# Performance work log

Measured on AMD Instinct MI355X. Metric: run time of the kernel, lower is better.

## Reference

```python
import jax, jax.numpy as jnp
import numpy as np

B, T, F, U = 64, 512, 1024, 256


def setup_inputs() -> dict:
    key = jax.random.key(0)
    ks = jax.random.split(key, 9)
    x = jax.random.normal(ks[0], (B, T, F), dtype=jnp.float32)
    # variable-length sequences, zero-padded tail (Masking layer semantics)
    lengths = jax.random.randint(ks[1], (B,), T // 2, T + 1)
    valid = (jnp.arange(T)[None, :] < lengths[:, None]).astype(jnp.float32)
    x = x * valid[:, :, None]
    s_fc = 1.0 / np.sqrt(F)
    s_u = 1.0 / np.sqrt(U)
    W_fc = jax.random.uniform(ks[2], (F, U), jnp.float32, -s_fc, s_fc)
    b_fc = jnp.zeros((U,), jnp.float32)
    W_x = jax.random.uniform(ks[3], (U, 4 * U), jnp.float32, -s_u, s_u)
    W_h = jax.random.uniform(ks[4], (U, 4 * U), jnp.float32, -s_u, s_u)
    # Keras unit_forget_bias: ones for forget-gate slice, zeros elsewhere
    b_lstm = jnp.concatenate([jnp.zeros((U,)), jnp.ones((U,)), jnp.zeros((2 * U,))]).astype(jnp.float32)
    W_p = jax.random.uniform(ks[5], (U, 1), jnp.float32, -s_u, s_u)
    b_p = jnp.zeros((1,), jnp.float32)
    return {"inputs": x, "W_fc": W_fc, "b_fc": b_fc, "W_x": W_x,
            "W_h": W_h, "b_lstm": b_lstm, "W_p": W_p, "b_p": b_p}


def _forward(inputs, W_fc, b_fc, W_x, W_h, b_lstm, W_p, b_p):
    # Masking layer: timestep masked iff ALL features == 0.0
    mask = jnp.any(inputs != 0.0, axis=-1)              # [B, T] bool
    x = inputs * mask[:, :, None].astype(inputs.dtype)  # Masking zeroes masked steps
    # Dense(units, relu) applied per timestep
    z = jax.nn.relu(jnp.einsum('btf,fu->btu', x, W_fc) + b_fc)  # [B, T, U]

    units = W_h.shape[0]
    h0 = jnp.zeros((x.shape[0], units), x.dtype)
    c0 = jnp.zeros((x.shape[0], units), x.dtype)

    def step(carry, xt_mt):
        h, c = carry
        xt, mt = xt_mt                                   # [B, U], [B]
        gates = xt @ W_x + h @ W_h + b_lstm              # [B, 4U]
        i, f, g, o = jnp.split(gates, 4, axis=-1)
        i = jax.nn.sigmoid(i)
        f = jax.nn.sigmoid(f)
        g = jnp.tanh(g)
        o = jax.nn.sigmoid(o)
        c_new = f * c + i * g
        h_new = o * jnp.tanh(c_new)
        m = mt[:, None]
        # Keras masked-RNN semantics: skip step, carry previous h/c and output
        h2 = jnp.where(m, h_new, h)
        c2 = jnp.where(m, c_new, c)
        return (h2, c2), h2

    z_t = jnp.swapaxes(z, 0, 1)        # [T, B, U]
    m_t = jnp.swapaxes(mask, 0, 1)     # [T, B]
    _, hs = jax.lax.scan(step, (h0, c0), (z_t, m_t))
    hs = jnp.swapaxes(hs, 0, 1)        # [B, T, U]
    # Dense(1, sigmoid) prediction head
    return jax.nn.sigmoid(jnp.einsum('btu,uo->bto', hs, W_p) + b_p)  # [B, T, 1]


def reference(inputs, W_fc, b_fc, W_x, W_h, b_lstm, W_p, b_p):
    return _forward(inputs, W_fc, b_fc, W_x, W_h, b_lstm, W_p, b_p)
```

## Files before the change

### kernel.cpp

```cpp
#include <hip/hip_runtime.h>
#include <hip/hip_fp16.h>
#include <hip/hip_fp8.h>
#include <cstdint>

#define BB 64
#define TT 512
#define FF 1024
#define UU 256
#define GG 1024

typedef _Float16 f16x8 __attribute__((ext_vector_type(8)));
typedef float f32x4 __attribute__((ext_vector_type(4)));
typedef int i32x8 __attribute__((ext_vector_type(8)));

typedef union { uint4 u4[2]; i32x8 v; } pk32;

__device__ __forceinline__ float sigmf_(float x) { return 1.f / (1.f + __expf(-x)); }
__device__ __forceinline__ float tanhf_(float x) { return 1.f - 2.f / (1.f + __expf(2.f * x)); }

__global__ __launch_bounds__(256) void mask_kernel(const float* __restrict__ x,
                                                   float* __restrict__ maskF) {
  int row = blockIdx.x;
  int tid = threadIdx.x;
  const float4* xr = (const float4*)(x + (size_t)row * FF);
  float4 v = xr[tid];
  bool nz = (v.x != 0.f) || (v.y != 0.f) || (v.z != 0.f) || (v.w != 0.f);
  __shared__ int flag;
  if (tid == 0) flag = 0;
  __syncthreads();
  if (__any(nz)) {
    if ((tid & 63) == 0) atomicOr(&flag, 1);
  }
  __syncthreads();
  if (tid == 0) maskF[row] = flag ? 1.f : 0.f;
}

__global__ __launch_bounds__(256) void pack_whP(const float* __restrict__ Wh,
                                                uint8_t* __restrict__ whP) {
  int col = blockIdx.x;
  int k = threadIdx.x;
  __hip_fp8_e4m3 f(Wh[(size_t)k * GG + col] * 16.f);
  whP[col * 256 + k] = (uint8_t)f.__x;
}

template <typename TA, bool RELU, bool PERM>
__global__ __launch_bounds__(256) void gemm16(const TA* __restrict__ A,
                                              const float* __restrict__ Bm,
                                              const float* __restrict__ bias,
                                              __half* __restrict__ C,
                                              int M, int N, int K) {
  __shared__ _Float16 As[128][40];
  __shared__ _Float16 Bs[64][40];
  int tid = threadIdx.x;
  int lane = tid & 63, w = tid >> 6;
  int wm = w & 1, wn = w >> 1;
  int m0 = blockIdx.x * 128, n0 = blockIdx.y * 64;
  int fr = lane & 15, ks = lane >> 4;

  f32x4 acc[4][2];
#pragma unroll
  for (int i = 0; i < 4; ++i)
#pragma unroll
    for (int j = 0; j < 2; ++j) acc[i][j] = (f32x4){0.f, 0.f, 0.f, 0.f};

  for (int k0 = 0; k0 < K; k0 += 32) {
    {
      int r = tid >> 3, kq = (tid & 7) * 4;
#pragma unroll
      for (int i = 0; i < 4; ++i) {
        int row = r + 32 * i;
        const TA* src = A + (size_t)(m0 + row) * K + k0 + kq;
        if constexpr (sizeof(TA) == 4) {
          float4 v = *reinterpret_cast<const float4*>(src);
          union { uint2 u; _Float16 h[4]; } pk;
          pk.h[0] = (_Float16)v.x; pk.h[1] = (_Float16)v.y;
          pk.h[2] = (_Float16)v.z; pk.h[3] = (_Float16)v.w;
          *reinterpret_cast<uint2*>(&As[row][kq]) = pk.u;
        } else {
          uint2 v = *reinterpret_cast<const uint2*>(src);
          *reinterpret_cast<uint2*>(&As[row][kq]) = v;
        }
      }
      int nn = tid & 63, kb = tid >> 6;
#pragma unroll
      for (int i = 0; i < 8; ++i) {
        int kk = kb + 4 * i;
        Bs[nn][kk] = (_Float16)Bm[(size_t)(k0 + kk) * N + n0 + nn];
      }
    }
    __syncthreads();
    f16x8 af[4], bf[2];
#pragma unroll
    for (int fm = 0; fm < 4; ++fm)
      af[fm] = *reinterpret_cast<const f16x8*>(&As[wm * 64 + fm * 16 + fr][ks * 8]);
#pragma unroll
    for (int fn = 0; fn < 2; ++fn)
      bf[fn] = *reinterpret_cast<const f16x8*>(&Bs[wn * 32 + fn * 16 + fr][ks * 8]);
#pragma unroll
    for (int fm = 0; fm < 4; ++fm)
#pragma unroll
      for (int fn = 0; fn < 2; ++fn)
        acc[fm][fn] = __builtin_amdgcn_mfma_f32_16x16x32_f16(af[fm], bf[fn], acc[fm][fn], 0, 0, 0);
    __syncthreads();
  }
#pragma unroll
  for (int fm = 0; fm < 4; ++fm)
#pragma unroll
    for (int fn = 0; fn < 2; ++fn) {
      int mg0 = m0 + wm * 64 + fm * 16 + ks * 4;
      int ng = n0 + wn * 32 + fn * 16 + fr;
      float bv = bias[ng];
      int ngs = PERM ? ((ng & 255) * 4 + (ng >> 8)) : ng;
#pragma unroll
      for (int r = 0; r < 4; ++r) {
        float v = acc[fm][fn][r] + bv;
        if constexpr (RELU) v = fmaxf(v, 0.f);
        C[(size_t)(mg0 + r) * N + ngs] = __float2half(v);
      }
    }
}

__attribute__((amdgpu_waves_per_eu(2, 2)))
__global__ void __launch_bounds__(512, 1)
lstm_rec(const uint8_t* __restrict__ whP,
         const __half* __restrict__ zxi,
         const float* __restrict__ maskF,
         const float* __restrict__ Wp,
         __half* __restrict__ ppG)
{
  __shared__ __align__(16) uint8_t hpk[2][256];
  __shared__ float mlds[TT];

  const int b = blockIdx.x;
  const int t = threadIdx.x;
  const int lane = t & 63, w = t >> 6;
  const int fr = lane & 15, q = lane >> 4;
  const int jj = q & 1;
  const int SC1 = 0x7F7F7F7F;

  const uint4* whP4 = (const uint4*)whP;

  pk32 bfr[2][8];
#pragma unroll
  for (int kt = 0; kt < 2; ++kt)
#pragma unroll
    for (int g = 0; g < 4; ++g)
#pragma unroll
      for (int j = 0; j < 2; ++j) {
        int col = g * 256 + w * 32 + j * 16 + fr;
        bfr[kt][g * 2 + j].u4[0] = whP4[col * 16 + kt * 8 + q * 2];
        bfr[kt][g * 2 + j].u4[1] = whP4[col * 16 + kt * 8 + q * 2 + 1];
      }
#pragma unroll
  for (int kt = 0; kt < 2; ++kt)
#pragma unroll
    for (int T = 0; T < 8; ++T) {
      asm volatile("" : "+v"(bfr[kt][T].u4[0].x), "+v"(bfr[kt][T].u4[0].y),
                        "+v"(bfr[kt][T].u4[0].z), "+v"(bfr[kt][T].u4[0].w));
      asm volatile("" : "+v"(bfr[kt][T].u4[1].x), "+v"(bfr[kt][T].u4[1].y),
                        "+v"(bfr[kt][T].u4[1].z), "+v"(bfr[kt][T].u4[1].w));
    }

  if (t < 64) ((uint32_t*)hpk[0])[t] = 0u;
  mlds[t] = maskF[b * TT + t];
  float c_state = 0.f, h_state = 0.f;
  const int ue = w * 32 + jj * 16 + fr;
  float wpv = Wp[ue];
  __syncthreads();

  const uint2* zp = (const uint2*)(zxi + (size_t)b * TT * GG);
  __half* ppp = ppG + (size_t)b * TT * UU;

  uint2 zx_c = zp[ue];
  __half pp_prev = __float2half(0.f);

  int p = 0;
  for (int step = 0; step < TT; ++step) {
    if (step > 0 && lane < 32) ppp[(size_t)(step - 1) * UU + w * 32 + lane] = pp_prev;

    const uint2* zq = zp + ((step + 1 < TT) ? 256 : 0);
    uint2 zx_n = zq[ue];
    float mval = mlds[step];

    const uint4* hp4 = (const uint4*)hpk[p];
    pk32 a0, a1;
    a0.u4[0] = hp4[q * 2];     a0.u4[1] = hp4[q * 2 + 1];
    a1.u4[0] = hp4[8 + q * 2]; a1.u4[1] = hp4[8 + q * 2 + 1];
    f32x4 d[8];
#pragma unroll
    for (int T = 0; T < 8; ++T) {
      f32x4 z = {0.f, 0.f, 0.f, 0.f};
      z = __builtin_amdgcn_mfma_scale_f32_16x16x128_f8f6f4(
          a0.v, bfr[0][T].v, z, 0, 0, 0, SC1, 0, SC1);
      d[T] = __builtin_amdgcn_mfma_scale_f32_16x16x128_f8f6f4(
          a1.v, bfr[1][T].v, z, 0, 0, 0, SC1, 0, SC1);
    }
    float s0 = d[0][0], s1 = d[1][0], s2 = d[2][0], s3 = d[3][0];
    float s4 = d[4][0], s5 = d[5][0], s6 = d[6][0], s7 = d[7][0];

    {
      union { uint2 u2; __half2 h2[2]; } zz;
      zz.u2 = zx_c;
      float2 zif = __half22float2(zz.h2[0]);
      float2 zgo = __half22float2(zz.h2[1]);
      float gi = fmaf(jj ? s1 : s0, 0.0625f, zif.x);
      float gf = fmaf(jj ? s3 : s2, 0.0625f, zif.y);
      float gg = fmaf(jj ? s5 : s4, 0.0625f, zgo.x);
      float go = fmaf(jj ? s7 : s6, 0.0625f, zgo.y);
      float ig = sigmf_(gi);
      float fg = sigmf_(gf);
      float g_ = tanhf_(gg);
      float og = sigmf_(go);
      float cn = fg * c_state + ig * g_;
      float hn = og * tanhf_(cn);
      bool on = (mval > 0.5f);
      c_state = on ? cn : c_state;
      h_state = on ? hn : h_state;
      __hip_fp8_e4m3 f8(h_state);
      if (lane < 32) hpk[p ^ 1][w * 32 + lane] = (uint8_t)f8.__x;
      pp_prev = __float2half(h_state * wpv);
    }
    asm volatile("s_waitcnt lgkmcnt(0)" ::: "memory");
    __builtin_amdgcn_s_barrier();
    asm volatile("" ::: "memory");
    p ^= 1;
    zp += 256;
    zx_c = zx_n;
  }
  if (lane < 32) ppp[(size_t)(TT - 1) * UU + w * 32 + lane] = pp_prev;
}

__global__ __launch_bounds__(256) void proj_kernel(const __half* __restrict__ ppG,
                                                   const float* __restrict__ bp,
                                                   float* __restrict__ out) {
  int row = blockIdx.x * 4 + (threadIdx.x >> 6);
  int lane = threadIdx.x & 63;
  const ushort4* pr = (const ushort4*)(ppG + (size_t)row * UU);
  ushort4 v = pr[lane];
  __half2 a = *reinterpret_cast<__half2*>(&v.x);
  __half2 c = *reinterpret_cast<__half2*>(&v.z);
  float2 af = __half22float2(a), cf = __half22float2(c);
  float s = af.x + af.y + cf.x + cf.y;
#pragma unroll
  for (int off = 32; off > 0; off >>= 1) s += __shfl_down(s, off);
  if (lane == 0) out[row] = 1.f / (1.f + __expf(-(s + bp[0])));
}

extern "C" void kernel_launch(void* const* d_in, const int* in_sizes, int n_in,
                              void* d_out, int out_size, void* d_ws, size_t ws_size,
                              hipStream_t stream) {
  const float* x = (const float*)d_in[0];
  const float* Wfc = (const float*)d_in[1];
  const float* bfc = (const float*)d_in[2];
  const float* Wx = (const float*)d_in[3];
  const float* Wh = (const float*)d_in[4];
  const float* blstm = (const float*)d_in[5];
  const float* Wp = (const float*)d_in[6];
  const float* bp = (const float*)d_in[7];
  float* out = (float*)d_out;

  char* ws = (char*)d_ws;
  float* maskF = (float*)(ws);
  __half* zh = (__half*)(ws + 131072);
  __half* zxi = (__half*)(ws + 131072 + 16777216);
  uint8_t* whP = (uint8_t*)(ws + 131072 + 16777216 + 67108864);
  __half* ppG = zh;

  mask_kernel<<<BB * TT, 256, 0, stream>>>(x, maskF);
  pack_whP<<<GG, 256, 0, stream>>>(Wh, whP);
  gemm16<float, true, false><<<dim3((BB * TT) / 128, UU / 64), 256, 0, stream>>>(
      x, Wfc, bfc, zh, BB * TT, UU, FF);
  gemm16<__half, false, true><<<dim3((BB * TT) / 128, GG / 64), 256, 0, stream>>>(
      zh, Wx, blstm, zxi, BB * TT, GG, UU);
  lstm_rec<<<BB, 512, 0, stream>>>(whP, zxi, maskF, Wp, ppG);
  proj_kernel<<<(BB * TT) / 4, 256, 0, stream>>>(ppG, bp, out);
}
```

Measured before the change: 666.8 us.

## Pack two batch rows per LSTM recurrence block into the MFMA M dimension

The recurrent kernel now has each 512-thread block process two sequences at once. Rows 0-7 of the 16-row MFMA A operand come from sequence A's hidden state and rows 8-15 from sequence B's, so the otherwise idle MFMA rows carry useful work. Each thread now computes the gate nonlinearities for two hidden units instead of one, and the grid shrinks to half as many blocks. The aim is to cut total recurrent work and block count. In exchange, per-step elementwise work roughly doubles on the serial critical path, and the device is left with fewer active CUs.

```diff
diff --git a/kernel.cpp b/kernel.cpp
--- a/kernel.cpp
+++ b/kernel.cpp
@@ -128,15 +128,18 @@
          const float* __restrict__ Wp,
          __half* __restrict__ ppG)
 {
-  __shared__ __align__(16) uint8_t hpk[2][256];
-  __shared__ float mlds[TT];
-
-  const int b = blockIdx.x;
+  __shared__ __align__(16) uint8_t hA[2][256];
+  __shared__ __align__(16) uint8_t hB[2][256];
+  __shared__ float mldsA[TT];
+  __shared__ float mldsB[TT];
+
+  const int b0 = blockIdx.x * 2, b1 = b0 + 1;
   const int t = threadIdx.x;
   const int lane = t & 63, w = t >> 6;
   const int fr = lane & 15, q = lane >> 4;
-  const int jj = q & 1;
   const int SC1 = 0x7F7F7F7F;
+  const bool isA = (q < 2);
+  const bool wr = ((q & 1) == 0);
 
   const uint4* whP4 = (const uint4*)whP;
 
@@ -161,31 +164,37 @@
                         "+v"(bfr[kt][T].u4[1].z), "+v"(bfr[kt][T].u4[1].w));
     }
 
-  if (t < 64) ((uint32_t*)hpk[0])[t] = 0u;
-  mlds[t] = maskF[b * TT + t];
-  float c_state = 0.f, h_state = 0.f;
-  const int ue = w * 32 + jj * 16 + fr;
-  float wpv = Wp[ue];
+  if (t < 64) { ((uint32_t*)hA[0])[t] = 0u; ((uint32_t*)hB[0])[t] = 0u; }
+  mldsA[t] = maskF[b0 * TT + t];
+  mldsB[t] = maskF[b1 * TT + t];
+
+  const int u0 = w * 32 + fr;
+  const int u1 = w * 32 + 16 + fr;
+  float c0 = 0.f, h0 = 0.f, c1 = 0.f, h1 = 0.f;
+  float wp0 = Wp[u0], wp1 = Wp[u1];
   __syncthreads();
 
-  const uint2* zp = (const uint2*)(zxi + (size_t)b * TT * GG);
-  __half* ppp = ppG + (size_t)b * TT * UU;
-
-  uint2 zx_c = zp[ue];
-  __half pp_prev = __float2half(0.f);
+  const int myb = isA ? b0 : b1;
+  const uint2* zp = (const uint2*)(zxi + (size_t)myb * TT * GG);
+  __half* ppp = ppG + (size_t)myb * TT * UU;
+
+  uint2 zx_c0 = zp[u0], zx_c1 = zp[u1];
+  __half pp0 = __float2half(0.f), pp1 = __float2half(0.f);
 
   int p = 0;
   for (int step = 0; step < TT; ++step) {
-    if (step > 0 && lane < 32) ppp[(size_t)(step - 1) * UU + w * 32 + lane] = pp_prev;
-
-    const uint2* zq = zp + ((step + 1 < TT) ? 256 : 0);
-    uint2 zx_n = zq[ue];
-    float mval = mlds[step];
-
-    const uint4* hp4 = (const uint4*)hpk[p];
+    if (step > 0 && wr) {
+      ppp[(size_t)(step - 1) * UU + u0] = pp0;
+      ppp[(size_t)(step - 1) * UU + u1] = pp1;
+    }
+    const uint2* zq = zp + ((step + 1 < TT) ? (size_t)(step + 1) * 256 : (size_t)step * 256);
+    uint2 zx_n0 = zq[u0], zx_n1 = zq[u1];
+    float mval = isA ? mldsA[step] : mldsB[step];
+
+    const uint4* hsrc = (const uint4*)((fr < 8) ? hA[p] : hB[p]);
     pk32 a0, a1;
-    a0.u4[0] = hp4[q * 2];     a0.u4[1] = hp4[q * 2 + 1];
-    a1.u4[0] = hp4[8 + q * 2]; a1.u4[1] = hp4[8 + q * 2 + 1];
+    a0.u4[0] = hsrc[q * 2];     a0.u4[1] = hsrc[q * 2 + 1];
+    a1.u4[0] = hsrc[8 + q * 2]; a1.u4[1] = hsrc[8 + q * 2 + 1];
     f32x4 d[8];
 #pragma unroll
     for (int T = 0; T < 8; ++T) {
@@ -195,39 +204,48 @@
       d[T] = __builtin_amdgcn_mfma_scale_f32_16x16x128_f8f6f4(
           a1.v, bfr[1][T].v, z, 0, 0, 0, SC1, 0, SC1);
     }
-    float s0 = d[0][0], s1 = d[1][0], s2 = d[2][0], s3 = d[3][0];
-    float s4 = d[4][0], s5 = d[5][0], s6 = d[6][0], s7 = d[7][0];
+    float si0 = d[0][0], si1 = d[1][0];
+    float sf0 = d[2][0], sf1 = d[3][0];
+    float sg0 = d[4][0], sg1 = d[5][0];
+    float so0 = d[6][0], so1 = d[7][0];
 
     {
-      union { uint2 u2; __half2 h2[2]; } zz;
-      zz.u2 = zx_c;
-      float2 zif = __half22float2(zz.h2[0]);
-      float2 zgo = __half22float2(zz.h2[1]);
-      float gi = fmaf(jj ? s1 : s0, 0.0625f, zif.x);
-      float gf = fmaf(jj ? s3 : s2, 0.0625f, zif.y);
-      float gg = fmaf(jj ? s5 : s4, 0.0625f, zgo.x);
-      float go = fmaf(jj ? s7 : s6, 0.0625f, zgo.y);
-      float ig = sigmf_(gi);
-      float fg = sigmf_(gf);
-      float g_ = tanhf_(gg);
-      float og = sigmf_(go);
-      float cn = fg * c_state + ig * g_;
-      float hn = og * tanhf_(cn);
+      union { uint2 u2; __half2 h2[2]; } za, zb;
+      za.u2 = zx_c0; zb.u2 = zx_c1;
+      float2 zif0 = __half22float2(za.h2[0]), zgo0 = __half22float2(za.h2[1]);
+      float2 zif1 = __half22float2(zb.h2[0]), zgo1 = __half22float2(zb.h2[1]);
+      float gi0 = fmaf(si0, 0.0625f, zif0.x), gi1 = fmaf(si1, 0.0625f, zif1.x);
+      float gf0 = fmaf(sf0, 0.0625f, zif0.y), gf1 = fmaf(sf1, 0.0625f, zif1.y);
+      float gg0 = fmaf(sg0, 0.0625f, zgo0.x), gg1 = fmaf(sg1, 0.0625f, zgo1.x);
+      float go0 = fmaf(so0, 0.0625f, zgo0.y), go1 = fmaf(so1, 0.0625f, zgo1.y);
+      float ig0 = sigmf_(gi0), ig1 = sigmf_(gi1);
+      float fg0 = sigmf_(gf0), fg1 = sigmf_(gf1);
+      float g_0 = tanhf_(gg0), g_1 = tanhf_(gg1);
+      float og0 = sigmf_(go0), og1 = sigmf_(go1);
+      float cn0 = fg0 * c0 + ig0 * g_0, cn1 = fg1 * c1 + ig1 * g_1;
+      float hn0 = og0 * tanhf_(cn0), hn1 = og1 * tanhf_(cn1);
       bool on = (mval > 0.5f);
-      c_state = on ? cn : c_state;
-      h_state = on ? hn : h_state;
-      __hip_fp8_e4m3 f8(h_state);
-      if (lane < 32) hpk[p ^ 1][w * 32 + lane] = (uint8_t)f8.__x;
-      pp_prev = __float2half(h_state * wpv);
+      c0 = on ? cn0 : c0; h0 = on ? hn0 : h0;
+      c1 = on ? cn1 : c1; h1 = on ? hn1 : h1;
+      __hip_fp8_e4m3 f80(h0), f81(h1);
+      if (wr) {
+        uint8_t* hdst = isA ? hA[p ^ 1] : hB[p ^ 1];
+        hdst[u0] = (uint8_t)f80.__x;
+        hdst[u1] = (uint8_t)f81.__x;
+      }
+      pp0 = __float2half(h0 * wp0);
+      pp1 = __float2half(h1 * wp1);
     }
     asm volatile("s_waitcnt lgkmcnt(0)" ::: "memory");
     __builtin_amdgcn_s_barrier();
     asm volatile("" ::: "memory");
     p ^= 1;
-    zp += 256;
-    zx_c = zx_n;
-  }
-  if (lane < 32) ppp[(size_t)(TT - 1) * UU + w * 32 + lane] = pp_prev;
+    zx_c0 = zx_n0; zx_c1 = zx_n1;
+  }
+  if (wr) {
+    ppp[(size_t)(TT - 1) * UU + u0] = pp0;
+    ppp[(size_t)(TT - 1) * UU + u1] = pp1;
+  }
 }
 
 __global__ __launch_bounds__(256) void proj_kernel(const __half* __restrict__ ppG,
@@ -272,6 +290,6 @@
       x, Wfc, bfc, zh, BB * TT, UU, FF);
   gemm16<__half, false, true><<<dim3((BB * TT) / 128, GG / 64), 256, 0, stream>>>(
       zh, Wx, blstm, zxi, BB * TT, GG, UU);
-  lstm_rec<<<BB, 512, 0, stream>>>(whP, zxi, maskF, Wp, ppG);
+  lstm_rec<<<BB / 2, 512, 0, stream>>>(whP, zxi, maskF, Wp, ppG);
   proj_kernel<<<(BB * TT) / 4, 256, 0, stream>>>(ppG, bp, out);
 }
```

After: 807.8 us. 21.1% more time.
